# Performance work log

Hardware: AMD Instinct MI355X
Metric: run time of the kernel (lower is better)

Reference implementation:

```python
import jax, jax.numpy as jnp
import numpy as np

H, W, NB, BS, D = 128, 256, 8, 96, 768
HIDDEN = 4 * D
LAMBDA = 0.01  # softshrink lambda (sparsity)
EPS = 1e-5     # torch LayerNorm default eps


def layernorm(x, g, b):
    mu = jnp.mean(x, axis=-1, keepdims=True)
    var = jnp.mean((x - mu) ** 2, axis=-1, keepdims=True)
    return (x - mu) * jax.lax.rsqrt(var + EPS) * g + b


def softshrink(x, lam):
    return jnp.sign(x) * jnp.maximum(jnp.abs(x) - lam, 0.0)


def afno(x, w1, w2, b1, b2):
    # x: [B, H*W, D]; bias branch is zeros since Block constructs AFNO with bias=None
    B, HW, Dd = x.shape
    xg = x.reshape(B, H, W, Dd)
    xf = jnp.fft.rfft2(xg, axes=(1, 2), norm='ortho')          # [B, H, W//2+1, D] complex
    xf = xf.reshape(B, H, W // 2 + 1, NB, BS)
    xr, xi = jnp.real(xf), jnp.imag(xf)

    def mul(t, w):  # block-diagonal channel mixing: [..., l, m] x [l, m, n]
        return jnp.einsum('bhwlm,lmn->bhwln', t, w)

    r1 = jax.nn.relu(mul(xr, w1[0]) - mul(xi, w1[1]) + b1[0])
    i1 = jax.nn.relu(mul(xr, w1[1]) + mul(xi, w1[0]) + b1[1])
    r2 = jax.nn.relu(mul(r1, w2[0]) - mul(i1, w2[1]) + b2[0])
    i2 = jax.nn.relu(mul(r1, w2[1]) + mul(i1, w2[0]) + b2[1])
    r2 = softshrink(r2, LAMBDA)
    i2 = softshrink(i2, LAMBDA)
    xc = (r2 + 1j * i2).reshape(B, H, W // 2 + 1, Dd)
    out = jnp.fft.irfft2(xc, s=(H, W), axes=(1, 2), norm='ortho')
    return out.reshape(B, HW, Dd)


def setup_inputs() -> dict:
    key = jax.random.key(0)
    ks = jax.random.split(key, 12)
    s = 0.02
    inp = {
        'x': jax.random.normal(ks[0], (2, H * W, D), dtype=jnp.float32),
        'norm1_g': jnp.ones((D,), jnp.float32),
        'norm1_b': jnp.zeros((D,), jnp.float32),
        'w1': s * jax.random.normal(ks[1], (2, NB, BS, BS), jnp.float32),
        'w2': s * jax.random.normal(ks[2], (2, NB, BS, BS), jnp.float32),
        'b1': s * jax.random.normal(ks[3], (2, NB, BS), jnp.float32),
        'b2': s * jax.random.normal(ks[4], (2, NB, BS), jnp.float32),
        'norm2_g': jnp.ones((D,), jnp.float32),
        'norm2_b': jnp.zeros((D,), jnp.float32),
        'fc1_w': s * jax.random.normal(ks[5], (D, HIDDEN), jnp.float32),
        'fc1_b': s * jax.random.normal(ks[6], (HIDDEN,), jnp.float32),
        'fc2_w': s * jax.random.normal(ks[7], (HIDDEN, D), jnp.float32),
        'fc2_b': s * jax.random.normal(ks[8], (D,), jnp.float32),
    }
    return inp


def reference(x, norm1_g, norm1_b, w1, w2, b1, b2, norm2_g, norm2_b,
              fc1_w, fc1_b, fc2_w, fc2_b):
    residual = x
    h = layernorm(x, norm1_g, norm1_b)
    h = afno(h, w1, w2, b1, b2)          # AFNO adds zero bias internally (bias=None)
    h = layernorm(h, norm2_g, norm2_b)
    h = jax.nn.gelu(h @ fc1_w + fc1_b, approximate=False)  # torch nn.GELU default = exact erf
    h = h @ fc2_w + fc2_b
    return h + residual
```

## Files before the change

### kernel.cpp

```cpp
#include <hip/hip_runtime.h>
#include <math.h>

#define Hh 128
#define Ww 256
#define Dd 768
#define NPLANE 256
#define WF 129
#define SFREQ (WF*Dd)
#define NPOS (2*Hh*WF)
#define LAMBDA_SS 0.01f

typedef short short8 __attribute__((ext_vector_type(8)));
typedef float floatx4 __attribute__((ext_vector_type(4)));

__device__ __forceinline__ float bf2f(ushort u) {
    union { unsigned int i; float f; } v; v.i = ((unsigned int)u) << 16; return v.f;
}
__device__ __forceinline__ ushort f2bf(float f) {
    union { float f; unsigned int i; } v; v.f = f;
    unsigned int r = v.i + 0x7fffu + ((v.i >> 16) & 1u);
    return (ushort)(r >> 16);
}
__device__ __forceinline__ short8 neg8(short8 a) {
    union { short8 s; unsigned int u[4]; } v; v.s = a;
    v.u[0] ^= 0x80008000u; v.u[1] ^= 0x80008000u;
    v.u[2] ^= 0x80008000u; v.u[3] ^= 0x80008000u;
    return v.s;
}

__global__ __launch_bounds__(256) void ln_kernel(const float* __restrict__ x,
        const float* __restrict__ g, const float* __restrict__ b,
        ushort* __restrict__ out) {
    int row = blockIdx.x;
    int tid = threadIdx.x;
    const float* xr = x + (size_t)row * Dd;
    float v0 = xr[tid], v1 = xr[tid + 256], v2 = xr[tid + 512];
    __shared__ float red[256];
    red[tid] = v0 + v1 + v2;
    __syncthreads();
    for (int o = 128; o > 0; o >>= 1) { if (tid < o) red[tid] += red[tid + o]; __syncthreads(); }
    float mean = red[0] * (1.0f / 768.0f);
    __syncthreads();
    float d0 = v0 - mean, d1 = v1 - mean, d2 = v2 - mean;
    red[tid] = d0 * d0 + d1 * d1 + d2 * d2;
    __syncthreads();
    for (int o = 128; o > 0; o >>= 1) { if (tid < o) red[tid] += red[tid + o]; __syncthreads(); }
    float inv = rsqrtf(red[0] * (1.0f / 768.0f) + 1e-5f);
    ushort* orow = out + (size_t)row * Dd;
    orow[tid]       = f2bf(d0 * inv * g[tid]       + b[tid]);
    orow[tid + 256] = f2bf(d1 * inv * g[tid + 256] + b[tid + 256]);
    orow[tid + 512] = f2bf(d2 * inv * g[tid + 512] + b[tid + 512]);
}

#define TW_WFC_H  0
#define TW_WFC_L  65536
#define TW_WFS_H  131072
#define TW_WFS_L  196608
#define TW_HC_H   262144
#define TW_HC_L   278528
#define TW_HS_H   294912
#define TW_HS_L   311296
#define TW_HSN_H  327680
#define TW_HSN_L  344064
#define TW_WIC_H  360448
#define TW_WIC_L  401408
#define TW_WISN_H 442368
#define TW_WISN_L 483328
#define TW_TOTAL  524288

__device__ __forceinline__ void split_bf(float v, ushort* hi, ushort* lo) {
    ushort h = f2bf(v);
    *hi = h;
    *lo = f2bf(v - bf2f(h));
}

__global__ __launch_bounds__(256) void twiddle_prep_kernel(ushort* __restrict__ tw) {
    int fam = blockIdx.y;
    int idx = blockIdx.x * 256 + threadIdx.x;
    if (fam == 0) {
        if (idx >= 65536) return;
        int wf = idx >> 8, w = idx & 255;
        float c = 0.0f, s = 0.0f;
        if (wf < WF) {
            int t = (w * wf) & 255;
            float ang = (float)t * (float)(2.0 * M_PI / 256.0);
            c = cosf(ang) * 0.0625f;
            s = -sinf(ang) * 0.0625f;
        }
        split_bf(c, &tw[TW_WFC_H + idx], &tw[TW_WFC_L + idx]);
        split_bf(s, &tw[TW_WFS_H + idx], &tw[TW_WFS_L + idx]);
    } else if (fam == 1) {
        if (idx >= 16384) return;
        int a = idx >> 7, b = idx & 127;
        int t = (a * b) & 127;
        float ang = (float)t * (float)(2.0 * M_PI / 128.0);
        const float sc = 0.08838834764831845f;
        float c = cosf(ang) * sc, s = sinf(ang) * sc;
        split_bf(c,  &tw[TW_HC_H + idx],  &tw[TW_HC_L + idx]);
        split_bf(s,  &tw[TW_HS_H + idx],  &tw[TW_HS_L + idx]);
        split_bf(-s, &tw[TW_HSN_H + idx], &tw[TW_HSN_L + idx]);
    } else {
        if (idx >= 40960) return;
        int w = idx / 160, wf = idx - w * 160;
        float c = 0.0f, s = 0.0f;
        if (wf < WF) {
            int t = (w * wf) & 255;
            float ang = (float)t * (float)(2.0 * M_PI / 256.0);
            float wt = (wf == 0 || wf == 128) ? 0.5f : 1.0f;
            c = wt * cosf(ang) * 0.125f;
            s = -wt * sinf(ang) * 0.125f;
        }
        split_bf(c, &tw[TW_WIC_H + idx],  &tw[TW_WIC_L + idx]);
        split_bf(s, &tw[TW_WISN_H + idx], &tw[TW_WISN_L + idx]);
    }
}

__global__ __launch_bounds__(256) void transpose_bf_kernel(const ushort* __restrict__ in,
        ushort* __restrict__ out, int R, int C, int Rpad, size_t inB, size_t outB) {
    __shared__ ushort tile[32][33];
    int z = blockIdx.z;
    int c0 = blockIdx.x * 32, r0 = blockIdx.y * 32;
    int tx = threadIdx.x, ty = threadIdx.y;
    const ushort* ip = in + (size_t)z * inB;
    ushort* op = out + (size_t)z * outB;
    for (int j = 0; j < 32; j += 8) {
        int r = r0 + ty + j;
        tile[ty + j][tx] = (r < R) ? ip[(size_t)r * C + c0 + tx] : (ushort)0;
    }
    __syncthreads();
    for (int j = 0; j < 32; j += 8)
        op[(size_t)(c0 + ty + j) * Rpad + r0 + tx] = tile[tx][ty + j];
}

#define CSTR 144
__global__ __launch_bounds__(256, 2) void dftc_kernel(
        const ushort* __restrict__ A1h, const ushort* __restrict__ A1l,
        const ushort* __restrict__ A2h, const ushort* __restrict__ A2l,
        const ushort* __restrict__ B1, const ushort* __restrict__ B2,
        ushort* __restrict__ O1, ushort* __restrict__ O2,
        int M, int N, int K, size_t strideB, size_t strideC, int mode) {
    __shared__ __align__(16) ushort smem[128 * CSTR];
    ushort* Bs1 = smem;
    ushort* Bs2 = smem + 5120;
    int tid = threadIdx.x;
    int bn = blockIdx.x * 128, bm = blockIdx.y * 128;
    int z = blockIdx.z;
    const ushort* b1g = B1 + (size_t)z * strideB;
    const ushort* b2g = B2 + (size_t)z * strideB;
    int wave = tid >> 6, lane = tid & 63;
    int wy = wave >> 1, wx = wave & 1;
    int quad = lane >> 4, l16 = lane & 15;
    int sr = tid >> 2, sc = (tid & 3) * 8;

    size_t arow = (size_t)(bm + wy * 64 + l16) * K + quad * 8;
    const ushort* a1h_p = A1h + arow;
    const ushort* a1l_p = A1l + arow;
    const ushort* a2h_p = A2h + arow;
    const ushort* a2l_p = A2l + arow;

    floatx4 acc1[4][4], acc2[4][4];
#pragma unroll
    for (int i = 0; i < 4; ++i)
#pragma unroll
        for (int j = 0; j < 4; ++j) {
            acc1[i][j][0] = 0.f; acc1[i][j][1] = 0.f; acc1[i][j][2] = 0.f; acc1[i][j][3] = 0.f;
            acc2[i][j][0] = 0.f; acc2[i][j][1] = 0.f; acc2[i][j][2] = 0.f; acc2[i][j][3] = 0.f;
        }

    for (int k0 = 0; k0 < K; k0 += 32) {
        uint4 b1a = *(const uint4*)(b1g + (size_t)(bn + sr) * K + k0 + sc);
        uint4 b1b = *(const uint4*)(b1g + (size_t)(bn + sr + 64) * K + k0 + sc);
        uint4 b2a, b2b;
        if (mode) {
            b2a = *(const uint4*)(b2g + (size_t)(bn + sr) * K + k0 + sc);
            b2b = *(const uint4*)(b2g + (size_t)(bn + sr + 64) * K + k0 + sc);
        }
        __syncthreads();
        *(uint4*)&Bs1[sr * 40 + sc] = b1a;
        *(uint4*)&Bs1[(sr + 64) * 40 + sc] = b1b;
        if (mode) {
            *(uint4*)&Bs2[sr * 40 + sc] = b2a;
            *(uint4*)&Bs2[(sr + 64) * 40 + sc] = b2b;
        }
        __syncthreads();
        short8 bf1[4], bf2[4];
#pragma unroll
        for (int j = 0; j < 4; ++j)
            bf1[j] = *(const short8*)&Bs1[(wx * 64 + j * 16 + l16) * 40 + quad * 8];
        if (mode) {
#pragma unroll
            for (int j = 0; j < 4; ++j)
                bf2[j] = *(const short8*)&Bs2[(wx * 64 + j * 16 + l16) * 40 + quad * 8];
        }
#pragma unroll
        for (int i = 0; i < 4; ++i) {
            size_t ao = (size_t)i * 16 * K + k0;
            short8 a1h_ = *(const short8*)(a1h_p + ao);
            short8 a1l_ = *(const short8*)(a1l_p + ao);
            short8 a2h_ = *(const short8*)(a2h_p + ao);
            short8 a2l_ = *(const short8*)(a2l_p + ao);
            if (mode) {
#pragma unroll
                for (int j = 0; j < 4; ++j) {
                    acc1[i][j] = __builtin_amdgcn_mfma_f32_16x16x32_bf16(a1h_, bf1[j], acc1[i][j], 0, 0, 0);
                    acc1[i][j] = __builtin_amdgcn_mfma_f32_16x16x32_bf16(a1l_, bf1[j], acc1[i][j], 0, 0, 0);
                    acc1[i][j] = __builtin_amdgcn_mfma_f32_16x16x32_bf16(a2h_, bf2[j], acc1[i][j], 0, 0, 0);
                    acc1[i][j] = __builtin_amdgcn_mfma_f32_16x16x32_bf16(a2l_, bf2[j], acc1[i][j], 0, 0, 0);
                }
                short8 n2h = neg8(a2h_), n2l = neg8(a2l_);
#pragma unroll
                for (int j = 0; j < 4; ++j) {
                    acc2[i][j] = __builtin_amdgcn_mfma_f32_16x16x32_bf16(a1h_, bf2[j], acc2[i][j], 0, 0, 0);
                    acc2[i][j] = __builtin_amdgcn_mfma_f32_16x16x32_bf16(a1l_, bf2[j], acc2[i][j], 0, 0, 0);
                    acc2[i][j] = __builtin_amdgcn_mfma_f32_16x16x32_bf16(n2h, bf1[j], acc2[i][j], 0, 0, 0);
                    acc2[i][j] = __builtin_amdgcn_mfma_f32_16x16x32_bf16(n2l, bf1[j], acc2[i][j], 0, 0, 0);
                }
            } else {
#pragma unroll
                for (int j = 0; j < 4; ++j) {
                    acc1[i][j] = __builtin_amdgcn_mfma_f32_16x16x32_bf16(a1h_, bf1[j], acc1[i][j], 0, 0, 0);
                    acc1[i][j] = __builtin_amdgcn_mfma_f32_16x16x32_bf16(a1l_, bf1[j], acc1[i][j], 0, 0, 0);
                    acc2[i][j] = __builtin_amdgcn_mfma_f32_16x16x32_bf16(a2h_, bf1[j], acc2[i][j], 0, 0, 0);
                    acc2[i][j] = __builtin_amdgcn_mfma_f32_16x16x32_bf16(a2l_, bf1[j], acc2[i][j], 0, 0, 0);
                }
            }
        }
    }

    int srow = tid >> 4;
    int schunk = (tid & 15) * 8;
#pragma unroll
    for (int half = 0; half < 2; ++half) {
        ushort* Optr = half ? O2 : O1;
        __syncthreads();
#pragma unroll
        for (int i = 0; i < 4; ++i) {
            int r0 = (wy * 64 + i * 16 + quad * 4) * CSTR;
#pragma unroll
            for (int j = 0; j < 4; ++j) {
                int cc = wx * 64 + j * 16 + l16;
#pragma unroll
                for (int r = 0; r < 4; ++r) {
                    float v = half ? acc2[i][j][r] : acc1[i][j][r];
                    smem[r0 + r * CSTR + cc] = f2bf(v);
                }
            }
        }
        __syncthreads();
#pragma unroll
        for (int p = 0; p < 8; ++p) {
            int row = p * 16 + srow;
            int grow = bm + row;
            if (grow < M) {
                uint4 v = *(const uint4*)&smem[row * CSTR + schunk];
                *(uint4*)&Optr[(size_t)z * strideC + (size_t)grow * N + bn + schunk] = v;
            }
        }
    }
}

__global__ __launch_bounds__(256, 2) void dftwi_kernel(
        const ushort* __restrict__ A1h, const ushort* __restrict__ A1l,
        const ushort* __restrict__ A2h, const ushort* __restrict__ A2l,
        const ushort* __restrict__ B1, const ushort* __restrict__ B2,
        float* __restrict__ O, int M, int N, int K, size_t strideB, size_t strideC) {
    __shared__ __align__(16) ushort smem[128 * CSTR];
    ushort* Bs1 = smem;
    ushort* Bs2 = smem + 5120;
    float* Csf = (float*)smem;
    int tid = threadIdx.x;
    int bn = blockIdx.x * 128, bm = blockIdx.y * 128;
    int z = blockIdx.z;
    const ushort* b1g = B1 + (size_t)z * strideB;
    const ushort* b2g = B2 + (size_t)z * strideB;
    int wave = tid >> 6, lane = tid & 63;
    int wy = wave >> 1, wx = wave & 1;
    int quad = lane >> 4, l16 = lane & 15;
    int sr = tid >> 2, sc = (tid & 3) * 8;

    size_t arow = (size_t)(bm + wy * 64 + l16) * K + quad * 8;
    const ushort* a1h_p = A1h + arow;
    const ushort* a1l_p = A1l + arow;
    const ushort* a2h_p = A2h + arow;
    const ushort* a2l_p = A2l + arow;

    floatx4 acc[4][4];
#pragma unroll
    for (int i = 0; i < 4; ++i)
#pragma unroll
        for (int j = 0; j < 4; ++j) { acc[i][j][0] = 0.f; acc[i][j][1] = 0.f; acc[i][j][2] = 0.f; acc[i][j][3] = 0.f; }

    for (int k0 = 0; k0 < K; k0 += 32) {
        uint4 b1a = *(const uint4*)(b1g + (size_t)(bn + sr) * K + k0 + sc);
        uint4 b1b = *(const uint4*)(b1g + (size_t)(bn + sr + 64) * K + k0 + sc);
        uint4 b2a = *(const uint4*)(b2g + (size_t)(bn + sr) * K + k0 + sc);
        uint4 b2b = *(const uint4*)(b2g + (size_t)(bn + sr + 64) * K + k0 + sc);
        __syncthreads();
        *(uint4*)&Bs1[sr * 40 + sc] = b1a;
        *(uint4*)&Bs1[(sr + 64) * 40 + sc] = b1b;
        *(uint4*)&Bs2[sr * 40 + sc] = b2a;
        *(uint4*)&Bs2[(sr + 64) * 40 + sc] = b2b;
        __syncthreads();
        short8 bf1[4], bf2[4];
#pragma unroll
        for (int j = 0; j < 4; ++j) {
            bf1[j] = *(const short8*)&Bs1[(wx * 64 + j * 16 + l16) * 40 + quad * 8];
            bf2[j] = *(const short8*)&Bs2[(wx * 64 + j * 16 + l16) * 40 + quad * 8];
        }
#pragma unroll
        for (int i = 0; i < 4; ++i) {
            size_t ao = (size_t)i * 16 * K + k0;
            short8 a1h_ = *(const short8*)(a1h_p + ao);
            short8 a1l_ = *(const short8*)(a1l_p + ao);
            short8 a2h_ = *(const short8*)(a2h_p + ao);
            short8 a2l_ = *(const short8*)(a2l_p + ao);
#pragma unroll
            for (int j = 0; j < 4; ++j) {
                acc[i][j] = __builtin_amdgcn_mfma_f32_16x16x32_bf16(a1h_, bf1[j], acc[i][j], 0, 0, 0);
                acc[i][j] = __builtin_amdgcn_mfma_f32_16x16x32_bf16(a1l_, bf1[j], acc[i][j], 0, 0, 0);
                acc[i][j] = __builtin_amdgcn_mfma_f32_16x16x32_bf16(a2h_, bf2[j], acc[i][j], 0, 0, 0);
                acc[i][j] = __builtin_amdgcn_mfma_f32_16x16x32_bf16(a2l_, bf2[j], acc[i][j], 0, 0, 0);
            }
        }
    }

    int srow = tid >> 5;
    int chunk = (tid & 31) * 4;
#pragma unroll
    for (int h = 0; h < 2; ++h) {
        __syncthreads();
        if (wy == h) {
#pragma unroll
            for (int i = 0; i < 4; ++i) {
                int r0 = (i * 16 + quad * 4) * CSTR;
#pragma unroll
                for (int j = 0; j < 4; ++j) {
                    int cc = wx * 64 + j * 16 + l16;
#pragma unroll
                    for (int r = 0; r < 4; ++r)
                        Csf[r0 + r * CSTR + cc] = acc[i][j][r];
                }
            }
        }
        __syncthreads();
#pragma unroll
        for (int p = 0; p < 8; ++p) {
            int row = p * 8 + srow;
            uint4 v = *(const uint4*)&Csf[row * CSTR + chunk];
            *(uint4*)&O[(size_t)z * strideC + (size_t)(bm + h * 64 + row) * N + bn + chunk] = v;
        }
    }
}

__global__ __launch_bounds__(256) void wmix_prep_kernel(const float* __restrict__ w,
        ushort* __restrict__ wt) {
    int mat = blockIdx.x;
    const float* src = w + (size_t)mat * 96 * 96;
    ushort* dst = wt + (size_t)mat * 96 * 96;
    for (int idx = threadIdx.x; idx < 96 * 96; idx += 256) {
        int n = idx / 96, m = idx - n * 96;
        dst[idx] = f2bf(src[(size_t)m * 96 + n]);
    }
}

#define WSTR 104
__global__ __launch_bounds__(256) void mix_mfma_kernel(const ushort* __restrict__ Xr,
        const ushort* __restrict__ Xi, const ushort* __restrict__ Wt,
        const float* __restrict__ bias, ushort* __restrict__ Or,
        ushort* __restrict__ Oi, int shrink) {
    int l = blockIdx.y;
    int bm = blockIdx.x * 128;
    int tid = threadIdx.x;
    int wv = tid >> 6, lane = tid & 63;
    int quad = lane >> 4, l16 = lane & 15;

    __shared__ __align__(16) ushort Wr_s[96 * WSTR];
    __shared__ __align__(16) ushort Wi_s[96 * WSTR];
    const ushort* wr_g = Wt + (size_t)l * 96 * 96;
    const ushort* wi_g = Wt + (size_t)(8 + l) * 96 * 96;
    for (int idx = tid; idx < (96 * 96) / 4; idx += 256) {
        int n = idx / 24, mq = idx - n * 24;
        *(uint2*)&Wr_s[n * WSTR + mq * 4] = *(const uint2*)(wr_g + (size_t)n * 96 + mq * 4);
        *(uint2*)&Wi_s[n * WSTR + mq * 4] = *(const uint2*)(wi_g + (size_t)n * 96 + mq * 4);
    }

    floatx4 accr[2][6], acci[2][6];
#pragma unroll
    for (int i = 0; i < 2; ++i)
#pragma unroll
        for (int j = 0; j < 6; ++j) {
            accr[i][j][0] = 0.f; accr[i][j][1] = 0.f; accr[i][j][2] = 0.f; accr[i][j][3] = 0.f;
            acci[i][j][0] = 0.f; acci[i][j][1] = 0.f; acci[i][j][2] = 0.f; acci[i][j][3] = 0.f;
        }

    int row = bm + wv * 32 + l16;
    const ushort* agr = Xr + (size_t)row * 768 + l * 96;
    const ushort* agi = Xi + (size_t)row * 768 + l * 96;
    __syncthreads();

#pragma unroll
    for (int ks = 0; ks < 3; ++ks) {
        int ko = ks * 32 + quad * 8;
        short8 ar0 = *(const short8*)(agr + ko);
        short8 ar1 = *(const short8*)(agr + (size_t)16 * 768 + ko);
        short8 ai0 = *(const short8*)(agi + ko);
        short8 ai1 = *(const short8*)(agi + (size_t)16 * 768 + ko);
        short8 an0 = neg8(ai0), an1 = neg8(ai1);
#pragma unroll
        for (int j = 0; j < 6; ++j) {
            short8 br = *(const short8*)&Wr_s[(j * 16 + l16) * WSTR + ko];
            short8 bi = *(const short8*)&Wi_s[(j * 16 + l16) * WSTR + ko];
            accr[0][j] = __builtin_amdgcn_mfma_f32_16x16x32_bf16(ar0, br, accr[0][j], 0, 0, 0);
            accr[0][j] = __builtin_amdgcn_mfma_f32_16x16x32_bf16(an0, bi, accr[0][j], 0, 0, 0);
            acci[0][j] = __builtin_amdgcn_mfma_f32_16x16x32_bf16(ar0, bi, acci[0][j], 0, 0, 0);
            acci[0][j] = __builtin_amdgcn_mfma_f32_16x16x32_bf16(ai0, br, acci[0][j], 0, 0, 0);
            accr[1][j] = __builtin_amdgcn_mfma_f32_16x16x32_bf16(ar1, br, accr[1][j], 0, 0, 0);
            accr[1][j] = __builtin_amdgcn_mfma_f32_16x16x32_bf16(an1, bi, accr[1][j], 0, 0, 0);
            acci[1][j] = __builtin_amdgcn_mfma_f32_16x16x32_bf16(ar1, bi, acci[1][j], 0, 0, 0);
            acci[1][j] = __builtin_amdgcn_mfma_f32_16x16x32_bf16(ai1, br, acci[1][j], 0, 0, 0);
        }
    }

#pragma unroll
    for (int i = 0; i < 2; ++i) {
        int row0 = bm + wv * 32 + i * 16 + quad * 4;
#pragma unroll
        for (int j = 0; j < 6; ++j) {
            int col = j * 16 + l16;
            float bvr = bias[l * 96 + col];
            float bvi = bias[768 + l * 96 + col];
#pragma unroll
            for (int r = 0; r < 4; ++r) {
                float vr = accr[i][j][r] + bvr;
                float vi = acci[i][j][r] + bvi;
                if (shrink) { vr = fmaxf(vr - LAMBDA_SS, 0.0f); vi = fmaxf(vi - LAMBDA_SS, 0.0f); }
                else        { vr = fmaxf(vr, 0.0f);             vi = fmaxf(vi, 0.0f); }
                size_t o = (size_t)(row0 + r) * 768 + l * 96 + col;
                Or[o] = f2bf(vr);
                Oi[o] = f2bf(vi);
            }
        }
    }
}

__global__ __launch_bounds__(256) void transpose_kernel(const float* __restrict__ in,
        ushort* __restrict__ out, int R, int C) {
    __shared__ float tile[32][33];
    int c0 = blockIdx.x * 32, r0 = blockIdx.y * 32;
    int tx = threadIdx.x, ty = threadIdx.y;
    for (int j = 0; j < 32; j += 8)
        tile[ty + j][tx] = in[(size_t)(r0 + ty + j) * C + c0 + tx];
    __syncthreads();
    for (int j = 0; j < 32; j += 8)
        out[(size_t)(c0 + ty + j) * R + r0 + tx] = f2bf(tile[tx][ty + j]);
}

#define GBM 128
#define GBN 128
#define GBK 32
__global__ __launch_bounds__(256) void gemm_bt_kernel(const ushort* __restrict__ A,
        const ushort* __restrict__ Bt, void* __restrict__ Cv, int M, int N, int K,
        const float* __restrict__ bias, const float* __restrict__ resid,
        int act, int out_f32) {
    __shared__ __align__(16) ushort As[GBM * GBK];
    __shared__ __align__(16) ushort Bs[GBN * GBK];
    int tid = threadIdx.x;
    int bm = blockIdx.y * GBM, bn = blockIdx.x * GBN;
    int wave = tid >> 6, lane = tid & 63;
    int wy = wave >> 1, wx = wave & 1;
    int quad = lane >> 4, l16 = lane & 15;
    int sr = tid >> 2;
    int sc = (tid & 3) * 8;
    const ushort* Ag = A + (size_t)(bm + sr) * K + sc;
    const ushort* Bg = Bt + (size_t)(bn + sr) * K + sc;

    floatx4 acc[4][4];
#pragma unroll
    for (int i = 0; i < 4; ++i)
#pragma unroll
        for (int j = 0; j < 4; ++j) { acc[i][j][0] = 0.f; acc[i][j][1] = 0.f; acc[i][j][2] = 0.f; acc[i][j][3] = 0.f; }

    for (int k0 = 0; k0 < K; k0 += GBK) {
        uint4 a0 = *(const uint4*)(Ag + k0);
        uint4 a1 = *(const uint4*)(Ag + (size_t)64 * K + k0);
        uint4 b0 = *(const uint4*)(Bg + k0);
        uint4 b1 = *(const uint4*)(Bg + (size_t)64 * K + k0);
        __syncthreads();
        *(uint4*)&As[sr * GBK + sc] = a0;
        *(uint4*)&As[(sr + 64) * GBK + sc] = a1;
        *(uint4*)&Bs[sr * GBK + sc] = b0;
        *(uint4*)&Bs[(sr + 64) * GBK + sc] = b1;
        __syncthreads();
        short8 af[4], bfv[4];
#pragma unroll
        for (int i = 0; i < 4; ++i)
            af[i] = *(const short8*)&As[(wy * 64 + i * 16 + l16) * GBK + quad * 8];
#pragma unroll
        for (int j = 0; j < 4; ++j)
            bfv[j] = *(const short8*)&Bs[(wx * 64 + j * 16 + l16) * GBK + quad * 8];
#pragma unroll
        for (int i = 0; i < 4; ++i)
#pragma unroll
            for (int j = 0; j < 4; ++j)
                acc[i][j] = __builtin_amdgcn_mfma_f32_16x16x32_bf16(af[i], bfv[j], acc[i][j], 0, 0, 0);
    }

#pragma unroll
    for (int i = 0; i < 4; ++i) {
        int row0 = bm + wy * 64 + i * 16 + quad * 4;
#pragma unroll
        for (int j = 0; j < 4; ++j) {
            int col = bn + wx * 64 + j * 16 + l16;
            float bv = bias ? bias[col] : 0.0f;
#pragma unroll
            for (int r = 0; r < 4; ++r) {
                float v = acc[i][j][r] + bv;
                if (act == 1) v = 0.5f * v * (1.0f + erff(v * 0.70710678118f));
                size_t o = (size_t)(row0 + r) * N + col;
                if (out_f32) {
                    float vv = v + (resid ? resid[o] : 0.0f);
                    ((float*)Cv)[o] = vv;
                } else {
                    ((ushort*)Cv)[o] = f2bf(v);
                }
            }
        }
    }
}

extern "C" void kernel_launch(void* const* d_in, const int* in_sizes, int n_in,
                              void* d_out, int out_size, void* d_ws, size_t ws_size,
                              hipStream_t stream) {
    const float* x    = (const float*)d_in[0];
    const float* n1g  = (const float*)d_in[1];
    const float* n1b  = (const float*)d_in[2];
    const float* w1   = (const float*)d_in[3];
    const float* w2   = (const float*)d_in[4];
    const float* b1   = (const float*)d_in[5];
    const float* b2   = (const float*)d_in[6];
    const float* n2g  = (const float*)d_in[7];
    const float* n2b  = (const float*)d_in[8];
    const float* fc1w = (const float*)d_in[9];
    const float* fc1b = (const float*)d_in[10];
    const float* fc2w = (const float*)d_in[11];
    const float* fc2b = (const float*)d_in[12];
    float*  outf = (float*)d_out;
    ushort* outu = (ushort*)d_out;

    ushort* ws  = (ushort*)d_ws;
    ushort* W1t = ws;
    ushort* W2t = W1t + (size_t)3072 * 768;
    ushort* tw  = W2t + (size_t)768 * 3072;
    ushort* AR  = tw + TW_TOTAL;

    const size_t FSZ = (size_t)NPLANE * SFREQ;
    ushort* S1t = AR;
    ushort* FrT = AR;
    ushort* FiT = AR + FSZ;
    ushort* Mr  = AR;
    ushort* Mi  = AR + FSZ;
    ushort* NrT = AR;
    ushort* NiT = AR + FSZ;
    ushort* HrT = AR;
    ushort* HiT = AR + (size_t)256 * 768 * 160;
    ushort* Abf = AR;
    ushort* hid = AR + (size_t)65536 * 768;

    ushort* S1 = outu;
    ushort* Fr = outu;
    ushort* Fi = outu + FSZ;
    ushort* Gr = outu;
    ushort* Gi = outu + FSZ;
    ushort* Nr = outu;
    ushort* Ni = outu + FSZ;
    ushort* Hr = outu;
    ushort* Hi = outu + FSZ;
    ushort* W1mix = outu + 2 * FSZ;
    ushort* W2mix = W1mix + (size_t)2 * 8 * 96 * 96;

    transpose_kernel<<<dim3(3072 / 32, 768 / 32), dim3(32, 8), 0, stream>>>(fc1w, W1t, 768, 3072);
    transpose_kernel<<<dim3(768 / 32, 3072 / 32), dim3(32, 8), 0, stream>>>(fc2w, W2t, 3072, 768);
    wmix_prep_kernel<<<16, 256, 0, stream>>>(w1, W1mix);
    wmix_prep_kernel<<<16, 256, 0, stream>>>(w2, W2mix);
    twiddle_prep_kernel<<<dim3(256, 3), 256, 0, stream>>>(tw);

    ln_kernel<<<65536, 256, 0, stream>>>(x, n1g, n1b, S1);

    transpose_bf_kernel<<<dim3(768 / 32, 256 / 32, 256), dim3(32, 8), 0, stream>>>(
        S1, S1t, 256, 768, 256, (size_t)256 * 768, (size_t)768 * 256);
    dftc_kernel<<<dim3(768 / 128, 2, 256), 256, 0, stream>>>(
        tw + TW_WFC_H, tw + TW_WFC_L, tw + TW_WFS_H, tw + TW_WFS_L,
        S1t, S1t, Fr, Fi, WF, 768, 256, (size_t)768 * 256, (size_t)SFREQ, 0);

    transpose_bf_kernel<<<dim3(SFREQ / 32, 128 / 32, 2), dim3(32, 8), 0, stream>>>(
        Fr, FrT, 128, SFREQ, 128, (size_t)128 * SFREQ, (size_t)128 * SFREQ);
    transpose_bf_kernel<<<dim3(SFREQ / 32, 128 / 32, 2), dim3(32, 8), 0, stream>>>(
        Fi, FiT, 128, SFREQ, 128, (size_t)128 * SFREQ, (size_t)128 * SFREQ);
    dftc_kernel<<<dim3(SFREQ / 128, 1, 2), 256, 0, stream>>>(
        tw + TW_HC_H, tw + TW_HC_L, tw + TW_HS_H, tw + TW_HS_L,
        FrT, FiT, Gr, Gi, 128, SFREQ, 128, (size_t)128 * SFREQ, (size_t)128 * SFREQ, 1);

    mix_mfma_kernel<<<dim3(NPOS / 128, 8), 256, 0, stream>>>(Gr, Gi, W1mix, b1, Mr, Mi, 0);
    mix_mfma_kernel<<<dim3(NPOS / 128, 8), 256, 0, stream>>>(Mr, Mi, W2mix, b2, Nr, Ni, 1);

    transpose_bf_kernel<<<dim3(SFREQ / 32, 128 / 32, 2), dim3(32, 8), 0, stream>>>(
        Nr, NrT, 128, SFREQ, 128, (size_t)128 * SFREQ, (size_t)128 * SFREQ);
    transpose_bf_kernel<<<dim3(SFREQ / 32, 128 / 32, 2), dim3(32, 8), 0, stream>>>(
        Ni, NiT, 128, SFREQ, 128, (size_t)128 * SFREQ, (size_t)128 * SFREQ);
    dftc_kernel<<<dim3(SFREQ / 128, 1, 2), 256, 0, stream>>>(
        tw + TW_HC_H, tw + TW_HC_L, tw + TW_HS_H, tw + TW_HS_L,
        NiT, NrT, Hi, Hr, 128, SFREQ, 128, (size_t)128 * SFREQ, (size_t)128 * SFREQ, 1);

    transpose_bf_kernel<<<dim3(768 / 32, 5, 256), dim3(32, 8), 0, stream>>>(
        Hr, HrT, WF, 768, 160, (size_t)SFREQ, (size_t)768 * 160);
    transpose_bf_kernel<<<dim3(768 / 32, 5, 256), dim3(32, 8), 0, stream>>>(
        Hi, HiT, WF, 768, 160, (size_t)SFREQ, (size_t)768 * 160);
    dftwi_kernel<<<dim3(768 / 128, 2, 256), 256, 0, stream>>>(
        tw + TW_WIC_H, tw + TW_WIC_L, tw + TW_WISN_H, tw + TW_WISN_L,
        HrT, HiT, outf, 256, 768, 160, (size_t)768 * 160, (size_t)256 * 768);

    ln_kernel<<<65536, 256, 0, stream>>>(outf, n2g, n2b, Abf);

    const int CH = 8192;
    for (int c = 0; c < 8; ++c) {
        const ushort* Aln = Abf + (size_t)c * CH * 768;
        gemm_bt_kernel<<<dim3(3072 / GBN, CH / GBM), 256, 0, stream>>>(
            Aln, W1t, hid, CH, 3072, 768, fc1b, nullptr, 1, 0);
        gemm_bt_kernel<<<dim3(768 / GBN, CH / GBM), 256, 0, stream>>>(
            hid, W2t, outf + (size_t)c * CH * 768, CH, 768, 3072, fc2b,
            x + (size_t)c * CH * 768, 0, 1);
    }
}
```

Measured before the change: 2.991 ms.

## Use direct global-to-LDS loads in GEMM/DFT kernels and widen transpose tiles

```diff
diff --git a/kernel.cpp b/kernel.cpp
--- a/kernel.cpp
+++ b/kernel.cpp
@@ -26,6 +26,11 @@
     v.u[0] ^= 0x80008000u; v.u[1] ^= 0x80008000u;
     v.u[2] ^= 0x80008000u; v.u[3] ^= 0x80008000u;
     return v.s;
+}
+__device__ __forceinline__ void gload_lds16(const ushort* g, ushort* l) {
+    __builtin_amdgcn_global_load_lds(
+        (const __attribute__((address_space(1))) unsigned int*)g,
+        (__attribute__((address_space(3))) unsigned int*)l, 16, 0, 0);
 }
 
 __global__ __launch_bounds__(256) void ln_kernel(const float* __restrict__ x,
@@ -117,40 +122,52 @@
 
 __global__ __launch_bounds__(256) void transpose_bf_kernel(const ushort* __restrict__ in,
         ushort* __restrict__ out, int R, int C, int Rpad, size_t inB, size_t outB) {
-    __shared__ ushort tile[32][33];
+    __shared__ ushort tile[64][66];
     int z = blockIdx.z;
-    int c0 = blockIdx.x * 32, r0 = blockIdx.y * 32;
+    int c0 = blockIdx.x * 64, r0 = blockIdx.y * 64;
     int tx = threadIdx.x, ty = threadIdx.y;
     const ushort* ip = in + (size_t)z * inB;
     ushort* op = out + (size_t)z * outB;
-    for (int j = 0; j < 32; j += 8) {
+#pragma unroll
+    for (int j = 0; j < 64; j += 8) {
         int r = r0 + ty + j;
-        tile[ty + j][tx] = (r < R) ? ip[(size_t)r * C + c0 + tx] : (ushort)0;
+        uint v = 0;
+        if (r < R) v = *(const uint*)&ip[(size_t)r * C + c0 + tx * 2];
+        *(uint*)&tile[ty + j][tx * 2] = v;
     }
     __syncthreads();
-    for (int j = 0; j < 32; j += 8)
-        op[(size_t)(c0 + ty + j) * Rpad + r0 + tx] = tile[tx][ty + j];
-}
-
-#define CSTR 144
+    int rr = tx * 2;
+#pragma unroll
+    for (int j = 0; j < 64; j += 8) {
+        int c = ty + j;
+        if (r0 + rr < Rpad) {
+            union { uint u; ushort s[2]; } v;
+            v.s[0] = tile[rr][c];
+            v.s[1] = tile[rr + 1][c];
+            *(uint*)&op[(size_t)(c0 + c) * Rpad + r0 + rr] = v.u;
+        }
+    }
+}
+
 __global__ __launch_bounds__(256, 2) void dftc_kernel(
         const ushort* __restrict__ A1h, const ushort* __restrict__ A1l,
         const ushort* __restrict__ A2h, const ushort* __restrict__ A2l,
         const ushort* __restrict__ B1, const ushort* __restrict__ B2,
         ushort* __restrict__ O1, ushort* __restrict__ O2,
         int M, int N, int K, size_t strideB, size_t strideC, int mode) {
-    __shared__ __align__(16) ushort smem[128 * CSTR];
+    __shared__ __align__(16) ushort smem[9216];
     ushort* Bs1 = smem;
-    ushort* Bs2 = smem + 5120;
+    ushort* Bs2 = smem + 4096;
     int tid = threadIdx.x;
     int bn = blockIdx.x * 128, bm = blockIdx.y * 128;
     int z = blockIdx.z;
-    const ushort* b1g = B1 + (size_t)z * strideB;
-    const ushort* b2g = B2 + (size_t)z * strideB;
-    int wave = tid >> 6, lane = tid & 63;
-    int wy = wave >> 1, wx = wave & 1;
+    int wv = tid >> 6, lane = tid & 63;
+    int wy = wv >> 1, wx = wv & 1;
     int quad = lane >> 4, l16 = lane & 15;
     int sr = tid >> 2, sc = (tid & 3) * 8;
+
+    const ushort* b1s = B1 + (size_t)z * strideB + (size_t)(bn + sr) * K + sc;
+    const ushort* b2s = B2 + (size_t)z * strideB + (size_t)(bn + sr) * K + sc;
 
     size_t arow = (size_t)(bm + wy * 64 + l16) * K + quad * 8;
     const ushort* a1h_p = A1h + arow;
@@ -168,29 +185,22 @@
         }
 
     for (int k0 = 0; k0 < K; k0 += 32) {
-        uint4 b1a = *(const uint4*)(b1g + (size_t)(bn + sr) * K + k0 + sc);
-        uint4 b1b = *(const uint4*)(b1g + (size_t)(bn + sr + 64) * K + k0 + sc);
-        uint4 b2a, b2b;
+        __syncthreads();
+        gload_lds16(b1s + k0, Bs1 + wv * 512);
+        gload_lds16(b1s + (size_t)64 * K + k0, Bs1 + 2048 + wv * 512);
         if (mode) {
-            b2a = *(const uint4*)(b2g + (size_t)(bn + sr) * K + k0 + sc);
-            b2b = *(const uint4*)(b2g + (size_t)(bn + sr + 64) * K + k0 + sc);
-        }
-        __syncthreads();
-        *(uint4*)&Bs1[sr * 40 + sc] = b1a;
-        *(uint4*)&Bs1[(sr + 64) * 40 + sc] = b1b;
+            gload_lds16(b2s + k0, Bs2 + wv * 512);
+            gload_lds16(b2s + (size_t)64 * K + k0, Bs2 + 2048 + wv * 512);
+        }
+        __syncthreads();
+        short8 bf1[4], bf2v[4];
+#pragma unroll
+        for (int j = 0; j < 4; ++j)
+            bf1[j] = *(const short8*)&Bs1[(wx * 64 + j * 16 + l16) * 32 + quad * 8];
         if (mode) {
-            *(uint4*)&Bs2[sr * 40 + sc] = b2a;
-            *(uint4*)&Bs2[(sr + 64) * 40 + sc] = b2b;
-        }
-        __syncthreads();
-        short8 bf1[4], bf2[4];
-#pragma unroll
-        for (int j = 0; j < 4; ++j)
-            bf1[j] = *(const short8*)&Bs1[(wx * 64 + j * 16 + l16) * 40 + quad * 8];
-        if (mode) {
 #pragma unroll
             for (int j = 0; j < 4; ++j)
-                bf2[j] = *(const short8*)&Bs2[(wx * 64 + j * 16 + l16) * 40 + quad * 8];
+                bf2v[j] = *(const short8*)&Bs2[(wx * 64 + j * 16 + l16) * 32 + quad * 8];
         }
 #pragma unroll
         for (int i = 0; i < 4; ++i) {
@@ -204,14 +214,14 @@
                 for (int j = 0; j < 4; ++j) {
                     acc1[i][j] = __builtin_amdgcn_mfma_f32_16x16x32_bf16(a1h_, bf1[j], acc1[i][j], 0, 0, 0);
                     acc1[i][j] = __builtin_amdgcn_mfma_f32_16x16x32_bf16(a1l_, bf1[j], acc1[i][j], 0, 0, 0);
-                    acc1[i][j] = __builtin_amdgcn_mfma_f32_16x16x32_bf16(a2h_, bf2[j], acc1[i][j], 0, 0, 0);
-                    acc1[i][j] = __builtin_amdgcn_mfma_f32_16x16x32_bf16(a2l_, bf2[j], acc1[i][j], 0, 0, 0);
+                    acc1[i][j] = __builtin_amdgcn_mfma_f32_16x16x32_bf16(a2h_, bf2v[j], acc1[i][j], 0, 0, 0);
+                    acc1[i][j] = __builtin_amdgcn_mfma_f32_16x16x32_bf16(a2l_, bf2v[j], acc1[i][j], 0, 0, 0);
                 }
                 short8 n2h = neg8(a2h_), n2l = neg8(a2l_);
 #pragma unroll
                 for (int j = 0; j < 4; ++j) {
-                    acc2[i][j] = __builtin_amdgcn_mfma_f32_16x16x32_bf16(a1h_, bf2[j], acc2[i][j], 0, 0, 0);
-                    acc2[i][j] = __builtin_amdgcn_mfma_f32_16x16x32_bf16(a1l_, bf2[j], acc2[i][j], 0, 0, 0);
+                    acc2[i][j] = __builtin_amdgcn_mfma_f32_16x16x32_bf16(a1h_, bf2v[j], acc2[i][j], 0, 0, 0);
+                    acc2[i][j] = __builtin_amdgcn_mfma_f32_16x16x32_bf16(a1l_, bf2v[j], acc2[i][j], 0, 0, 0);
                     acc2[i][j] = __builtin_amdgcn_mfma_f32_16x16x32_bf16(n2h, bf1[j], acc2[i][j], 0, 0, 0);
                     acc2[i][j] = __builtin_amdgcn_mfma_f32_16x16x32_bf16(n2l, bf1[j], acc2[i][j], 0, 0, 0);
                 }
@@ -231,29 +241,34 @@
     int schunk = (tid & 15) * 8;
 #pragma unroll
     for (int half = 0; half < 2; ++half) {
-        ushort* Optr = half ? O2 : O1;
-        __syncthreads();
-#pragma unroll
-        for (int i = 0; i < 4; ++i) {
-            int r0 = (wy * 64 + i * 16 + quad * 4) * CSTR;
-#pragma unroll
-            for (int j = 0; j < 4; ++j) {
-                int cc = wx * 64 + j * 16 + l16;
-#pragma unroll
-                for (int r = 0; r < 4; ++r) {
-                    float v = half ? acc2[i][j][r] : acc1[i][j][r];
-                    smem[r0 + r * CSTR + cc] = f2bf(v);
+#pragma unroll
+        for (int out = 0; out < 2; ++out) {
+            __syncthreads();
+            if (wy == half) {
+#pragma unroll
+                for (int i = 0; i < 4; ++i) {
+                    int r0 = (i * 16 + quad * 4) * 144;
+#pragma unroll
+                    for (int j = 0; j < 4; ++j) {
+                        int cc = wx * 64 + j * 16 + l16;
+#pragma unroll
+                        for (int r = 0; r < 4; ++r) {
+                            float v = out ? acc2[i][j][r] : acc1[i][j][r];
+                            smem[r0 + r * 144 + cc] = f2bf(v);
+                        }
+                    }
                 }
             }
-        }
-        __syncthreads();
-#pragma unroll
-        for (int p = 0; p < 8; ++p) {
-            int row = p * 16 + srow;
-            int grow = bm + row;
-            if (grow < M) {
-                uint4 v = *(const uint4*)&smem[row * CSTR + schunk];
-                *(uint4*)&Optr[(size_t)z * strideC + (size_t)grow * N + bn + schunk] = v;
+            __syncthreads();
+            ushort* Optr = out ? O2 : O1;
+#pragma unroll
+            for (int p = 0; p < 4; ++p) {
+                int row = p * 16 + srow;
+                int grow = bm + half * 64 + row;
+                if (grow < M) {
+                    uint4 v = *(const uint4*)&smem[row * 144 + schunk];
+                    *(uint4*)&Optr[(size_t)z * strideC + (size_t)grow * N + bn + schunk] = v;
+                }
             }
         }
     }
@@ -264,19 +279,20 @@
         const ushort* __restrict__ A2h, const ushort* __restrict__ A2l,
         const ushort* __restrict__ B1, const ushort* __restrict__ B2,
         float* __restrict__ O, int M, int N, int K, size_t strideB, size_t strideC) {
-    __shared__ __align__(16) ushort smem[128 * CSTR];
+    __shared__ __align__(16) ushort smem[9216];
     ushort* Bs1 = smem;
-    ushort* Bs2 = smem + 5120;
+    ushort* Bs2 = smem + 4096;
     float* Csf = (float*)smem;
     int tid = threadIdx.x;
     int bn = blockIdx.x * 128, bm = blockIdx.y * 128;
     int z = blockIdx.z;
-    const ushort* b1g = B1 + (size_t)z * strideB;
-    const ushort* b2g = B2 + (size_t)z * strideB;
-    int wave = tid >> 6, lane = tid & 63;
-    int wy = wave >> 1, wx = wave & 1;
+    int wv = tid >> 6, lane = tid & 63;
+    int wy = wv >> 1, wx = wv & 1;
     int quad = lane >> 4, l16 = lane & 15;
     int sr = tid >> 2, sc = (tid & 3) * 8;
+
+    const ushort* b1s = B1 + (size_t)z * strideB + (size_t)(bn + sr) * K + sc;
+    const ushort* b2s = B2 + (size_t)z * strideB + (size_t)(bn + sr) * K + sc;
 
     size_t arow = (size_t)(bm + wy * 64 + l16) * K + quad * 8;
     const ushort* a1h_p = A1h + arow;
@@ -291,21 +307,17 @@
         for (int j = 0; j < 4; ++j) { acc[i][j][0] = 0.f; acc[i][j][1] = 0.f; acc[i][j][2] = 0.f; acc[i][j][3] = 0.f; }
 
     for (int k0 = 0; k0 < K; k0 += 32) {
-        uint4 b1a = *(const uint4*)(b1g + (size_t)(bn + sr) * K + k0 + sc);
-        uint4 b1b = *(const uint4*)(b1g + (size_t)(bn + sr + 64) * K + k0 + sc);
-        uint4 b2a = *(const uint4*)(b2g + (size_t)(bn + sr) * K + k0 + sc);
-        uint4 b2b = *(const uint4*)(b2g + (size_t)(bn + sr + 64) * K + k0 + sc);
-        __syncthreads();
-        *(uint4*)&Bs1[sr * 40 + sc] = b1a;
-        *(uint4*)&Bs1[(sr + 64) * 40 + sc] = b1b;
-        *(uint4*)&Bs2[sr * 40 + sc] = b2a;
-        *(uint4*)&Bs2[(sr + 64) * 40 + sc] = b2b;
-        __syncthreads();
-        short8 bf1[4], bf2[4];
+        __syncthreads();
+        gload_lds16(b1s + k0, Bs1 + wv * 512);
+        gload_lds16(b1s + (size_t)64 * K + k0, Bs1 + 2048 + wv * 512);
+        gload_lds16(b2s + k0, Bs2 + wv * 512);
+        gload_lds16(b2s + (size_t)64 * K + k0, Bs2 + 2048 + wv * 512);
+        __syncthreads();
+        short8 bf1[4], bf2v[4];
 #pragma unroll
         for (int j = 0; j < 4; ++j) {
-            bf1[j] = *(const short8*)&Bs1[(wx * 64 + j * 16 + l16) * 40 + quad * 8];
-            bf2[j] = *(const short8*)&Bs2[(wx * 64 + j * 16 + l16) * 40 + quad * 8];
+            bf1[j] = *(const short8*)&Bs1[(wx * 64 + j * 16 + l16) * 32 + quad * 8];
+            bf2v[j] = *(const short8*)&Bs2[(wx * 64 + j * 16 + l16) * 32 + quad * 8];
         }
 #pragma unroll
         for (int i = 0; i < 4; ++i) {
@@ -318,36 +330,38 @@
             for (int j = 0; j < 4; ++j) {
                 acc[i][j] = __builtin_amdgcn_mfma_f32_16x16x32_bf16(a1h_, bf1[j], acc[i][j], 0, 0, 0);
                 acc[i][j] = __builtin_amdgcn_mfma_f32_16x16x32_bf16(a1l_, bf1[j], acc[i][j], 0, 0, 0);
-                acc[i][j] = __builtin_amdgcn_mfma_f32_16x16x32_bf16(a2h_, bf2[j], acc[i][j], 0, 0, 0);
-                acc[i][j] = __builtin_amdgcn_mfma_f32_16x16x32_bf16(a2l_, bf2[j], acc[i][j], 0, 0, 0);
+                acc[i][j] = __builtin_amdgcn_mfma_f32_16x16x32_bf16(a2h_, bf2v[j], acc[i][j], 0, 0, 0);
+                acc[i][j] = __builtin_amdgcn_mfma_f32_16x16x32_bf16(a2l_, bf2v[j], acc[i][j], 0, 0, 0);
             }
         }
     }
 
-    int srow = tid >> 5;
+    int srow8 = tid >> 5;
     int chunk = (tid & 31) * 4;
 #pragma unroll
-    for (int h = 0; h < 2; ++h) {
-        __syncthreads();
-        if (wy == h) {
-#pragma unroll
-            for (int i = 0; i < 4; ++i) {
-                int r0 = (i * 16 + quad * 4) * CSTR;
+    for (int q = 0; q < 4; ++q) {
+        __syncthreads();
+        if (wy == (q >> 1)) {
+            int ibase = (q & 1) * 2;
+#pragma unroll
+            for (int ii = 0; ii < 2; ++ii) {
+                int i = ibase + ii;
+                int r0 = (ii * 16 + quad * 4) * 132;
 #pragma unroll
                 for (int j = 0; j < 4; ++j) {
                     int cc = wx * 64 + j * 16 + l16;
 #pragma unroll
                     for (int r = 0; r < 4; ++r)
-                        Csf[r0 + r * CSTR + cc] = acc[i][j][r];
+                        Csf[r0 + r * 132 + cc] = acc[i][j][r];
                 }
             }
         }
         __syncthreads();
 #pragma unroll
-        for (int p = 0; p < 8; ++p) {
-            int row = p * 8 + srow;
-            uint4 v = *(const uint4*)&Csf[row * CSTR + chunk];
-            *(uint4*)&O[(size_t)z * strideC + (size_t)(bm + h * 64 + row) * N + bn + chunk] = v;
+        for (int p = 0; p < 4; ++p) {
+            int row = p * 8 + srow8;
+            uint4 v = *(const uint4*)&Csf[row * 132 + chunk];
+            *(uint4*)&O[(size_t)z * strideC + (size_t)(bm + q * 32 + row) * N + bn + chunk] = v;
         }
     }
 }
@@ -473,6 +487,10 @@
     int sc = (tid & 3) * 8;
     const ushort* Ag = A + (size_t)(bm + sr) * K + sc;
     const ushort* Bg = Bt + (size_t)(bn + sr) * K + sc;
+    ushort* AsW  = As + wave * 512;
+    ushort* AsW2 = As + 2048 + wave * 512;
+    ushort* BsW  = Bs + wave * 512;
+    ushort* BsW2 = Bs + 2048 + wave * 512;
 
     floatx4 acc[4][4];
 #pragma unroll
@@ -481,15 +499,11 @@
         for (int j = 0; j < 4; ++j) { acc[i][j][0] = 0.f; acc[i][j][1] = 0.f; acc[i][j][2] = 0.f; acc[i][j][3] = 0.f; }
 
     for (int k0 = 0; k0 < K; k0 += GBK) {
-        uint4 a0 = *(const uint4*)(Ag + k0);
-        uint4 a1 = *(const uint4*)(Ag + (size_t)64 * K + k0);
-        uint4 b0 = *(const uint4*)(Bg + k0);
-        uint4 b1 = *(const uint4*)(Bg + (size_t)64 * K + k0);
-        __syncthreads();
-        *(uint4*)&As[sr * GBK + sc] = a0;
-        *(uint4*)&As[(sr + 64) * GBK + sc] = a1;
-        *(uint4*)&Bs[sr * GBK + sc] = b0;
-        *(uint4*)&Bs[(sr + 64) * GBK + sc] = b1;
+        __syncthreads();
+        gload_lds16(Ag + k0, AsW);
+        gload_lds16(Ag + (size_t)64 * K + k0, AsW2);
+        gload_lds16(Bg + k0, BsW);
+        gload_lds16(Bg + (size_t)64 * K + k0, BsW2);
         __syncthreads();
         short8 af[4], bfv[4];
 #pragma unroll
@@ -586,15 +600,15 @@
 
     ln_kernel<<<65536, 256, 0, stream>>>(x, n1g, n1b, S1);
 
-    transpose_bf_kernel<<<dim3(768 / 32, 256 / 32, 256), dim3(32, 8), 0, stream>>>(
+    transpose_bf_kernel<<<dim3(768 / 64, 256 / 64, 256), dim3(32, 8), 0, stream>>>(
         S1, S1t, 256, 768, 256, (size_t)256 * 768, (size_t)768 * 256);
     dftc_kernel<<<dim3(768 / 128, 2, 256), 256, 0, stream>>>(
         tw + TW_WFC_H, tw + TW_WFC_L, tw + TW_WFS_H, tw + TW_WFS_L,
         S1t, S1t, Fr, Fi, WF, 768, 256, (size_t)768 * 256, (size_t)SFREQ, 0);
 
-    transpose_bf_kernel<<<dim3(SFREQ / 32, 128 / 32, 2), dim3(32, 8), 0, stream>>>(
+    transpose_bf_kernel<<<dim3(SFREQ / 64, 2, 2), dim3(32, 8), 0, stream>>>(
         Fr, FrT, 128, SFREQ, 128, (size_t)128 * SFREQ, (size_t)128 * SFREQ);
-    transpose_bf_kernel<<<dim3(SFREQ / 32, 128 / 32, 2), dim3(32, 8), 0, stream>>>(
+    transpose_bf_kernel<<<dim3(SFREQ / 64, 2, 2), dim3(32, 8), 0, stream>>>(
         Fi, FiT, 128, SFREQ, 128, (size_t)128 * SFREQ, (size_t)128 * SFREQ);
     dftc_kernel<<<dim3(SFREQ / 128, 1, 2), 256, 0, stream>>>(
         tw + TW_HC_H, tw + TW_HC_L, tw + TW_HS_H, tw + TW_HS_L,
@@ -603,17 +617,17 @@
     mix_mfma_kernel<<<dim3(NPOS / 128, 8), 256, 0, stream>>>(Gr, Gi, W1mix, b1, Mr, Mi, 0);
     mix_mfma_kernel<<<dim3(NPOS / 128, 8), 256, 0, stream>>>(Mr, Mi, W2mix, b2, Nr, Ni, 1);
 
-    transpose_bf_kernel<<<dim3(SFREQ / 32, 128 / 32, 2), dim3(32, 8), 0, stream>>>(
+    transpose_bf_kernel<<<dim3(SFREQ / 64, 2, 2), dim3(32, 8), 0, stream>>>(
         Nr, NrT, 128, SFREQ, 128, (size_t)128 * SFREQ, (size_t)128 * SFREQ);
-    transpose_bf_kernel<<<dim3(SFREQ / 32, 128 / 32, 2), dim3(32, 8), 0, stream>>>(
+    transpose_bf_kernel<<<dim3(SFREQ / 64, 2, 2), dim3(32, 8), 0, stream>>>(
         Ni, NiT, 128, SFREQ, 128, (size_t)128 * SFREQ, (size_t)128 * SFREQ);
     dftc_kernel<<<dim3(SFREQ / 128, 1, 2), 256, 0, stream>>>(
         tw + TW_HC_H, tw + TW_HC_L, tw + TW_HS_H, tw + TW_HS_L,
         NiT, NrT, Hi, Hr, 128, SFREQ, 128, (size_t)128 * SFREQ, (size_t)128 * SFREQ, 1);
 
-    transpose_bf_kernel<<<dim3(768 / 32, 5, 256), dim3(32, 8), 0, stream>>>(
+    transpose_bf_kernel<<<dim3(768 / 64, 3, 256), dim3(32, 8), 0, stream>>>(
         Hr, HrT, WF, 768, 160, (size_t)SFREQ, (size_t)768 * 160);
-    transpose_bf_kernel<<<dim3(768 / 32, 5, 256), dim3(32, 8), 0, stream>>>(
+    transpose_bf_kernel<<<dim3(768 / 64, 3, 256), dim3(32, 8), 0, stream>>>(
         Hi, HiT, WF, 768, 160, (size_t)SFREQ, (size_t)768 * 160);
     dftwi_kernel<<<dim3(768 / 128, 2, 256), 256, 0, stream>>>(
         tw + TW_WIC_H, tw + TW_WIC_L, tw + TW_WISN_H, tw + TW_WISN_L,
```

New measurement: 2.886 ms. -3.5%, faster.
